# Kernel optimization log

Hardware: AMD Instinct MI355X
Metric: run time of the kernel (lower is better)

Reference implementation:

```python
import jax, jax.numpy as jnp
import numpy as np

N_NODES = 50000
N_GRAPHS = 256

def _gcn_layer(h, src, dst, W, b, n_nodes):
    # GCNConv: linear transform, add self-loops, symmetric deg^-1/2 norm, scatter-add, bias
    h = h @ W  # [N, C_out]
    loop = jnp.arange(n_nodes, dtype=src.dtype)
    src_f = jnp.concatenate([src, loop])
    dst_f = jnp.concatenate([dst, loop])
    ones = jnp.ones_like(dst_f, dtype=h.dtype)
    deg = jax.ops.segment_sum(ones, dst_f, num_segments=n_nodes)  # includes self-loops
    dinv = jnp.where(deg > 0, jax.lax.rsqrt(deg), 0.0)
    norm = dinv[src_f] * dinv[dst_f]  # [E+N]
    msg = h[src_f] * norm[:, None]
    out = jax.ops.segment_sum(msg, dst_f, num_segments=n_nodes)
    return out + b


def setup_inputs() -> dict:
    key = jax.random.key(0)
    ks = jax.random.split(key, 12)
    d_in, d_hid, nhid, nout = 128, 128, 256, 768
    x = jax.random.normal(ks[0], (N_NODES, d_in), dtype=jnp.float32)
    edge_index = jax.random.randint(ks[1], (2, 800000), 0, N_NODES, dtype=jnp.int64)
    batch = jnp.sort(jax.random.randint(ks[2], (N_NODES,), 0, N_GRAPHS, dtype=jnp.int64))
    def lin(k, fan_in, fan_out):
        lim = 1.0 / np.sqrt(fan_in)
        kw, kb = jax.random.split(k)
        W = jax.random.uniform(kw, (fan_in, fan_out), jnp.float32, -lim, lim)
        b = jax.random.uniform(kb, (fan_out,), jnp.float32, -lim, lim)
        return W, b
    W1, b1 = lin(ks[3], d_in, d_hid)
    W2, b2 = lin(ks[4], d_hid, d_hid)
    W3, b3 = lin(ks[5], d_hid, d_hid)
    Wm1, bm1 = lin(ks[6], d_hid, nhid)
    Wm2, bm2 = lin(ks[7], nhid, nout)
    return {"x": x, "edge_index": edge_index, "batch": batch,
            "W1": W1, "b1": b1, "W2": W2, "b2": b2, "W3": W3, "b3": b3,
            "Wm1": Wm1, "bm1": bm1, "Wm2": Wm2, "bm2": bm2}


def reference(x, edge_index, batch, W1, b1, W2, b2, W3, b3, Wm1, bm1, Wm2, bm2):
    src, dst = edge_index[0], edge_index[1]
    n = x.shape[0]
    h = jax.nn.relu(_gcn_layer(x, src, dst, W1, b1, n))
    h = jax.nn.relu(_gcn_layer(h, src, dst, W2, b2, n))
    h = _gcn_layer(h, src, dst, W3, b3, n)  # no relu before pooling (matches source)
    # global mean pool over graphs
    sums = jax.ops.segment_sum(h, batch, num_segments=N_GRAPHS)
    cnts = jax.ops.segment_sum(jnp.ones((n,), h.dtype), batch, num_segments=N_GRAPHS)
    pooled = sums / jnp.clip(cnts, 1.0)[:, None]  # [G, d_hid]
    out = jax.nn.relu(pooled @ Wm1 + bm1)
    out = out @ Wm2 + bm2  # [G, nout]
    return out
```

## Files before the change

kernel.cpp:

```cpp
#include <hip/hip_runtime.h>
#include <hip/hip_bf16.h>

using bf16 = __hip_bfloat16;
typedef __attribute__((ext_vector_type(8))) short bf16x8;
typedef __attribute__((ext_vector_type(4))) float f32x4;
typedef unsigned short u16;

__device__ __forceinline__ float lo2f(unsigned u) { return __uint_as_float(u << 16); }
__device__ __forceinline__ float hi2f(unsigned u) { return __uint_as_float(u & 0xffff0000u); }
__device__ __forceinline__ unsigned pack_bf2(float a, float b) {
    bf16 t0 = __float2bfloat16(a), t1 = __float2bfloat16(b);
    return (unsigned)*(unsigned short*)&t0 | ((unsigned)*(unsigned short*)&t1 << 16);
}

#define CAP 64
#define NPART 8
#define NCHUNK 256
#define PF 8

__global__ __launch_bounds__(256)
void fill_pad(const int* __restrict__ ei, int E, int N,
              int* __restrict__ cursor, u16* __restrict__ colPad)
{
    int part  = blockIdx.x & (NPART - 1);
    int chunk = blockIdx.x >> 3;
    int lo = (int)(((long long)N * part) >> 3);
    int hi = (int)(((long long)N * (part + 1)) >> 3);
    int csz = (E + NCHUNK - 1) / NCHUNK;
    int beg = chunk * csz;
    int end = min(beg + csz, E);
    const int* __restrict__ dstp = ei + E;
    for (int e0 = beg + (int)threadIdx.x; e0 < end; e0 += 256 * PF) {
        int dv[PF];
#pragma unroll
        for (int j = 0; j < PF; ++j) {
            int e = e0 + j * 256;
            dv[j] = (e < end) ? __builtin_nontemporal_load(dstp + e) : -1;
        }
#pragma unroll
        for (int j = 0; j < PF; ++j) {
            if (dv[j] >= lo && dv[j] < hi) {
                int e = e0 + j * 256;
                int s = __builtin_nontemporal_load(ei + e);
                int p = atomicAdd(&cursor[dv[j]], 1);
                if (p < CAP) colPad[(dv[j] << 6) + p] = (u16)s;
            }
        }
    }
}

__global__ __launch_bounds__(256)
void dinv_gstart(const int* __restrict__ cursor, int N, float* __restrict__ dinv,
                 const int* __restrict__ batch, int* __restrict__ gstart, int G,
                 u16* __restrict__ colPad, unsigned* __restrict__ gzero)
{
    int i = blockIdx.x * 256 + threadIdx.x;
    if (i < 64) gzero[i] = 0u;
    if (i >= N) return;
    int c = min(cursor[i], CAP);
    dinv[i] = rsqrtf((float)(c + 1));
    int pe = (c + 31) & ~31;
    if (pe > CAP) pe = CAP;
    for (int p = c; p < pe; ++p) colPad[(i << 6) + p] = (u16)N;
    int b = batch[i];
    int bp = (i == 0) ? -1 : batch[i - 1];
    for (int q = bp + 1; q <= b; ++q) gstart[q] = i;
    if (i == N - 1)
        for (int q = b + 1; q <= G; ++q) gstart[q] = N;
}

#define LDK 136

__global__ __launch_bounds__(256)
void gemm1_f32(const float* __restrict__ x, const float* __restrict__ W,
               const float* __restrict__ dinv, int N, bf16* __restrict__ g,
               int tiles)
{
    __shared__ short Wt[128 * LDK];
    for (int i = threadIdx.x; i < 128 * 128; i += 256) {
        int k = i >> 7, n = i & 127;
        bf16 b = __float2bfloat16(W[i]);
        Wt[n * LDK + k] = *(short*)&b;
    }
    __syncthreads();

    int wave = threadIdx.x >> 6;
    int lane = threadIdx.x & 63;
    int ln   = lane & 15;
    int quad = lane >> 4;

    for (int t = blockIdx.x; t < tiles; t += gridDim.x) {
        int m0 = t * 64 + wave * 16;
        if (m0 >= N) continue;

        int row = m0 + ln;
        if (row >= N) row = N - 1;
        const float* hrow = x + (size_t)row * 128;

        bf16x8 a[4];
#pragma unroll
        for (int kk = 0; kk < 4; ++kk) {
            float4 f0 = *(const float4*)(hrow + kk * 32 + quad * 8);
            float4 f1 = *(const float4*)(hrow + kk * 32 + quad * 8 + 4);
            float fv[8] = {f0.x, f0.y, f0.z, f0.w, f1.x, f1.y, f1.z, f1.w};
#pragma unroll
            for (int j = 0; j < 8; ++j) {
                bf16 tb = __float2bfloat16(fv[j]);
                ((short*)&a[kk])[j] = *(short*)&tb;
            }
        }

        f32x4 c[8];
#pragma unroll
        for (int nt = 0; nt < 8; ++nt) c[nt] = (f32x4){0.f, 0.f, 0.f, 0.f};
#pragma unroll
        for (int kk = 0; kk < 4; ++kk)
#pragma unroll
            for (int nt = 0; nt < 8; ++nt) {
                bf16x8 b = *(const bf16x8*)&Wt[(nt * 16 + ln) * LDK + kk * 32 + quad * 8];
                c[nt] = __builtin_amdgcn_mfma_f32_16x16x32_bf16(a[kk], b, c[nt], 0, 0, 0);
            }
#pragma unroll
        for (int r = 0; r < 4; ++r) {
            int m = m0 + quad * 4 + r;
            if (m < N) {
                float dv = dinv[m];
#pragma unroll
                for (int nt = 0; nt < 8; ++nt) {
                    bf16 val = __float2bfloat16(c[nt][r] * dv);
                    ((unsigned short*)g)[(size_t)m * 128 + nt * 16 + ln] = *(unsigned short*)&val;
                }
            }
        }
    }
}

__global__ __launch_bounds__(256)
void gemm_mfma(const bf16* __restrict__ hin, const float* __restrict__ W,
               const float* __restrict__ dinv, int N, bf16* __restrict__ g,
               int tiles)
{
    __shared__ short Wt[128 * LDK];
    for (int i = threadIdx.x; i < 128 * 128; i += 256) {
        int k = i >> 7, n = i & 127;
        bf16 b = __float2bfloat16(W[i]);
        Wt[n * LDK + k] = *(short*)&b;
    }
    __syncthreads();

    int wave = threadIdx.x >> 6;
    int lane = threadIdx.x & 63;
    int ln   = lane & 15;
    int quad = lane >> 4;

    for (int t = blockIdx.x; t < tiles; t += gridDim.x) {
        int m0 = t * 64 + wave * 16;
        if (m0 >= N) continue;

        int row = m0 + ln;
        if (row >= N) row = N - 1;
        const short* hrow = (const short*)hin + (size_t)row * 128;

        bf16x8 a[4];
#pragma unroll
        for (int kk = 0; kk < 4; ++kk)
            a[kk] = *(const bf16x8*)(hrow + kk * 32 + quad * 8);

        f32x4 c[8];
#pragma unroll
        for (int nt = 0; nt < 8; ++nt) c[nt] = (f32x4){0.f, 0.f, 0.f, 0.f};
#pragma unroll
        for (int kk = 0; kk < 4; ++kk)
#pragma unroll
            for (int nt = 0; nt < 8; ++nt) {
                bf16x8 b = *(const bf16x8*)&Wt[(nt * 16 + ln) * LDK + kk * 32 + quad * 8];
                c[nt] = __builtin_amdgcn_mfma_f32_16x16x32_bf16(a[kk], b, c[nt], 0, 0, 0);
            }
#pragma unroll
        for (int r = 0; r < 4; ++r) {
            int m = m0 + quad * 4 + r;
            if (m < N) {
                float dv = dinv[m];
#pragma unroll
                for (int nt = 0; nt < 8; ++nt) {
                    bf16 val = __float2bfloat16(c[nt][r] * dv);
                    ((unsigned short*)g)[(size_t)m * 128 + nt * 16 + ln] = *(unsigned short*)&val;
                }
            }
        }
    }
}

__global__ __launch_bounds__(256)
void gather16(const bf16* __restrict__ g, const int* __restrict__ cnt,
              const u16* __restrict__ colPad, const float* __restrict__ dinv,
              const float* __restrict__ bias, int N, int do_relu, bf16* __restrict__ hout)
{
    int v = blockIdx.x * 4 + (threadIdx.x >> 6);
    if (v >= N) return;
    int lane = threadIdx.x & 63;
    const unsigned* gp = (const unsigned*)g;

    unsigned su = gp[(size_t)v * 64 + lane];
    float s0 = lo2f(su), s1 = hi2f(su);

    int beg = v << 6;
    int c = min(cnt[v], CAP);
    int pe = (c + 31) & ~31;
    if (pe > CAP) pe = CAP;
    int end = beg + pe;
    for (int i = beg; i < end; i += 32) {
        int4 cp0 = *(const int4*)(colPad + i);
        int4 cp1 = *(const int4*)(colPad + i + 8);
        int4 cp2 = *(const int4*)(colPad + i + 16);
        int4 cp3 = *(const int4*)(colPad + i + 24);
        int cc[32] = {
            cp0.x & 0xffff, (cp0.x >> 16) & 0xffff, cp0.y & 0xffff, (cp0.y >> 16) & 0xffff,
            cp0.z & 0xffff, (cp0.z >> 16) & 0xffff, cp0.w & 0xffff, (cp0.w >> 16) & 0xffff,
            cp1.x & 0xffff, (cp1.x >> 16) & 0xffff, cp1.y & 0xffff, (cp1.y >> 16) & 0xffff,
            cp1.z & 0xffff, (cp1.z >> 16) & 0xffff, cp1.w & 0xffff, (cp1.w >> 16) & 0xffff,
            cp2.x & 0xffff, (cp2.x >> 16) & 0xffff, cp2.y & 0xffff, (cp2.y >> 16) & 0xffff,
            cp2.z & 0xffff, (cp2.z >> 16) & 0xffff, cp2.w & 0xffff, (cp2.w >> 16) & 0xffff,
            cp3.x & 0xffff, (cp3.x >> 16) & 0xffff, cp3.y & 0xffff, (cp3.y >> 16) & 0xffff,
            cp3.z & 0xffff, (cp3.z >> 16) & 0xffff, cp3.w & 0xffff, (cp3.w >> 16) & 0xffff };
        unsigned uu[32];
#pragma unroll
        for (int j = 0; j < 32; ++j) uu[j] = gp[(size_t)cc[j] * 64 + lane];
#pragma unroll
        for (int j = 0; j < 32; ++j) { s0 += lo2f(uu[j]); s1 += hi2f(uu[j]); }
    }
    float dv = dinv[v];
    float2 bb = ((const float2*)bias)[lane];
    float r0 = fmaf(dv, s0, bb.x);
    float r1 = fmaf(dv, s1, bb.y);
    if (do_relu) { r0 = fmaxf(r0, 0.f); r1 = fmaxf(r1, 0.f); }
    ((unsigned*)hout)[(size_t)v * 64 + lane] = pack_bf2(r0, r1);
}

#define PCH 16
__global__ __launch_bounds__(64)
void pool_part(const bf16* __restrict__ h, const int* __restrict__ batch, int N,
               float* __restrict__ pooled)
{
    int c0 = blockIdx.x * PCH;
    if (c0 >= N) return;
    int t = threadIdx.x;
    int end = min(c0 + PCH, N);
    int cur = batch[c0];
    float a0 = 0.f, a1 = 0.f;
    const unsigned* hp = (const unsigned*)h;
    for (int v = c0; v < end; ++v) {
        int b = batch[v];
        if (b != cur) {
            atomicAdd(&pooled[cur * 128 + 2 * t], a0);
            atomicAdd(&pooled[cur * 128 + 2 * t + 1], a1);
            a0 = a1 = 0.f;
            cur = b;
        }
        unsigned u = hp[(size_t)v * 64 + t];
        a0 += lo2f(u);
        a1 += hi2f(u);
    }
    atomicAdd(&pooled[cur * 128 + 2 * t], a0);
    atomicAdd(&pooled[cur * 128 + 2 * t + 1], a1);
}

__global__ __launch_bounds__(256)
void mlp1g(const float* __restrict__ pooled, const int* __restrict__ gstart,
           const float* __restrict__ Wm1, const float* __restrict__ bm1,
           float* __restrict__ O)
{
    __shared__ float Ps[128];
    int gg = blockIdx.x, j = threadIdx.x;
    if (j < 128) {
        int c = gstart[gg + 1] - gstart[gg];
        Ps[j] = pooled[gg * 128 + j] / (float)(c > 0 ? c : 1);
    }
    __syncthreads();
    float s = 0.f;
#pragma unroll 4
    for (int k = 0; k < 128; ++k) s = fmaf(Ps[k], Wm1[k * 256 + j], s);
    O[(size_t)gg * 256 + j] = fmaxf(s + bm1[j], 0.f);
}

__global__ __launch_bounds__(768)
void mlp2g(const float* __restrict__ O, const float* __restrict__ Wm2,
           const float* __restrict__ bm2, float* __restrict__ out)
{
    __shared__ float Os[256];
    int gg = blockIdx.x, j = threadIdx.x;
    if (j < 256) Os[j] = O[(size_t)gg * 256 + j];
    __syncthreads();
    float s = 0.f;
#pragma unroll 4
    for (int k = 0; k < 256; ++k) s = fmaf(Os[k], Wm2[k * 768 + j], s);
    out[(size_t)gg * 768 + j] = s + bm2[j];
}

extern "C" void kernel_launch(void* const* d_in, const int* in_sizes, int n_in,
                              void* d_out, int out_size, void* d_ws, size_t ws_size,
                              hipStream_t stream)
{
    const float* x     = (const float*)d_in[0];
    const int*   ei    = (const int*)d_in[1];
    const int*   batch = (const int*)d_in[2];
    const float *W1 = (const float*)d_in[3],  *bb1 = (const float*)d_in[4];
    const float *W2 = (const float*)d_in[5],  *bb2 = (const float*)d_in[6];
    const float *W3 = (const float*)d_in[7],  *bb3 = (const float*)d_in[8];
    const float *Wm1 = (const float*)d_in[9],  *bm1 = (const float*)d_in[10];
    const float *Wm2 = (const float*)d_in[11], *bm2 = (const float*)d_in[12];

    const int N = in_sizes[2];
    const int E = in_sizes[1] / 2;
    const int G = out_size / 768;

    char* wp = (char*)d_ws;
    bf16* bufG   = (bf16*)wp;  wp += (size_t)(N + 1) * 128 * 2;
    bf16* bufH   = (bf16*)wp;  wp += (size_t)N * 128 * 2;
    u16*  colPad = (u16*)wp;   wp += (size_t)N * CAP * 2;
    int*  cursor = (int*)wp;   wp += (size_t)N * 4;
    float* pooled= (float*)wp; wp += (size_t)G * 128 * 4;
    float* dinv  = (float*)wp; wp += (size_t)N * 4;
    int*  gstart = (int*)wp;   wp += (size_t)(G + 1) * 4;
    float* Obuf  = (float*)wp; wp += (size_t)G * 256 * 4;

    hipMemsetAsync(cursor, 0, (size_t)N * 4 + (size_t)G * 128 * 4, stream);

    const int SB = (N + 255) / 256;
    const int gemm_tiles  = (N + 63) / 64;
    const int gemm_grid   = (gemm_tiles + 1) / 2;
    const int gather_grid = (N + 3) / 4;

    fill_pad<<<NPART * NCHUNK, 256, 0, stream>>>(ei, E, N, cursor, colPad);
    dinv_gstart<<<SB, 256, 0, stream>>>(cursor, N, dinv, batch, gstart, G,
                                        colPad, (unsigned*)bufG + (size_t)N * 64);

    gemm1_f32<<<gemm_grid, 256, 0, stream>>>(x, W1, dinv, N, bufG, gemm_tiles);
    gather16<<<gather_grid, 256, 0, stream>>>(bufG, cursor, colPad, dinv, bb1, N, 1, bufH);
    gemm_mfma<<<gemm_grid, 256, 0, stream>>>(bufH, W2, dinv, N, bufG, gemm_tiles);
    gather16<<<gather_grid, 256, 0, stream>>>(bufG, cursor, colPad, dinv, bb2, N, 1, bufH);
    gemm_mfma<<<gemm_grid, 256, 0, stream>>>(bufH, W3, dinv, N, bufG, gemm_tiles);
    gather16<<<gather_grid, 256, 0, stream>>>(bufG, cursor, colPad, dinv, bb3, N, 0, bufH);

    pool_part<<<(N + PCH - 1) / PCH, 64, 0, stream>>>(bufH, batch, N, pooled);
    mlp1g<<<G, 256, 0, stream>>>(pooled, gstart, Wm1, bm1, Obuf);
    mlp2g<<<G, 768, 0, stream>>>(Obuf, Wm2, bm2, (float*)d_out);
}
```

Baseline: 307.3 us.

## Fuse mean-pool into last gather and merge the two MLP kernels

The final gather now atomically adds each node's output directly into the per-graph pooled buffer instead of writing bf16 node features that a separate pool kernel re-reads. The two MLP head kernels are merged into one kernel, with the hidden activation kept in shared memory. This removes two launches, an intermediate buffer write/read and a global hidden buffer. In exchange, atomic traffic rises sharply (one atomic per node-feature instead of per 16-node chunk), with heavy contention on same-graph addresses.

```diff
diff --git a/kernel.cpp b/kernel.cpp
--- a/kernel.cpp
+++ b/kernel.cpp
@@ -194,7 +194,8 @@
 __global__ __launch_bounds__(256)
 void gather16(const bf16* __restrict__ g, const int* __restrict__ cnt,
               const u16* __restrict__ colPad, const float* __restrict__ dinv,
-              const float* __restrict__ bias, int N, int do_relu, bf16* __restrict__ hout)
+              const float* __restrict__ bias, int N, int do_relu, bf16* __restrict__ hout,
+              const int* __restrict__ batch, float* __restrict__ pooled, int do_pool)
 {
     int v = blockIdx.x * 4 + (threadIdx.x >> 6);
     if (v >= N) return;
@@ -234,62 +235,35 @@
     float r0 = fmaf(dv, s0, bb.x);
     float r1 = fmaf(dv, s1, bb.y);
     if (do_relu) { r0 = fmaxf(r0, 0.f); r1 = fmaxf(r1, 0.f); }
-    ((unsigned*)hout)[(size_t)v * 64 + lane] = pack_bf2(r0, r1);
-}
-
-#define PCH 16
-__global__ __launch_bounds__(64)
-void pool_part(const bf16* __restrict__ h, const int* __restrict__ batch, int N,
-               float* __restrict__ pooled)
-{
-    int c0 = blockIdx.x * PCH;
-    if (c0 >= N) return;
-    int t = threadIdx.x;
-    int end = min(c0 + PCH, N);
-    int cur = batch[c0];
-    float a0 = 0.f, a1 = 0.f;
-    const unsigned* hp = (const unsigned*)h;
-    for (int v = c0; v < end; ++v) {
+    if (do_pool) {
         int b = batch[v];
-        if (b != cur) {
-            atomicAdd(&pooled[cur * 128 + 2 * t], a0);
-            atomicAdd(&pooled[cur * 128 + 2 * t + 1], a1);
-            a0 = a1 = 0.f;
-            cur = b;
-        }
-        unsigned u = hp[(size_t)v * 64 + t];
-        a0 += lo2f(u);
-        a1 += hi2f(u);
-    }
-    atomicAdd(&pooled[cur * 128 + 2 * t], a0);
-    atomicAdd(&pooled[cur * 128 + 2 * t + 1], a1);
-}
-
-__global__ __launch_bounds__(256)
-void mlp1g(const float* __restrict__ pooled, const int* __restrict__ gstart,
-           const float* __restrict__ Wm1, const float* __restrict__ bm1,
-           float* __restrict__ O)
+        atomicAdd(&pooled[b * 128 + 2 * lane], r0);
+        atomicAdd(&pooled[b * 128 + 2 * lane + 1], r1);
+    } else {
+        ((unsigned*)hout)[(size_t)v * 64 + lane] = pack_bf2(r0, r1);
+    }
+}
+
+__global__ __launch_bounds__(768)
+void mlp_fused(const float* __restrict__ pooled, const int* __restrict__ gstart,
+               const float* __restrict__ Wm1, const float* __restrict__ bm1,
+               const float* __restrict__ Wm2, const float* __restrict__ bm2,
+               float* __restrict__ out)
 {
     __shared__ float Ps[128];
+    __shared__ float Os[256];
     int gg = blockIdx.x, j = threadIdx.x;
     if (j < 128) {
         int c = gstart[gg + 1] - gstart[gg];
         Ps[j] = pooled[gg * 128 + j] / (float)(c > 0 ? c : 1);
     }
     __syncthreads();
-    float s = 0.f;
+    if (j < 256) {
+        float s = 0.f;
 #pragma unroll 4
-    for (int k = 0; k < 128; ++k) s = fmaf(Ps[k], Wm1[k * 256 + j], s);
-    O[(size_t)gg * 256 + j] = fmaxf(s + bm1[j], 0.f);
-}
-
-__global__ __launch_bounds__(768)
-void mlp2g(const float* __restrict__ O, const float* __restrict__ Wm2,
-           const float* __restrict__ bm2, float* __restrict__ out)
-{
-    __shared__ float Os[256];
-    int gg = blockIdx.x, j = threadIdx.x;
-    if (j < 256) Os[j] = O[(size_t)gg * 256 + j];
+        for (int k = 0; k < 128; ++k) s = fmaf(Ps[k], Wm1[k * 256 + j], s);
+        Os[j] = fmaxf(s + bm1[j], 0.f);
+    }
     __syncthreads();
     float s = 0.f;
 #pragma unroll 4
@@ -322,7 +296,6 @@
     float* pooled= (float*)wp; wp += (size_t)G * 128 * 4;
     float* dinv  = (float*)wp; wp += (size_t)N * 4;
     int*  gstart = (int*)wp;   wp += (size_t)(G + 1) * 4;
-    float* Obuf  = (float*)wp; wp += (size_t)G * 256 * 4;
 
     hipMemsetAsync(cursor, 0, (size_t)N * 4 + (size_t)G * 128 * 4, stream);
 
@@ -336,13 +309,14 @@
                                         colPad, (unsigned*)bufG + (size_t)N * 64);
 
     gemm1_f32<<<gemm_grid, 256, 0, stream>>>(x, W1, dinv, N, bufG, gemm_tiles);
-    gather16<<<gather_grid, 256, 0, stream>>>(bufG, cursor, colPad, dinv, bb1, N, 1, bufH);
+    gather16<<<gather_grid, 256, 0, stream>>>(bufG, cursor, colPad, dinv, bb1, N, 1,
+                                              bufH, batch, pooled, 0);
     gemm_mfma<<<gemm_grid, 256, 0, stream>>>(bufH, W2, dinv, N, bufG, gemm_tiles);
-    gather16<<<gather_grid, 256, 0, stream>>>(bufG, cursor, colPad, dinv, bb2, N, 1, bufH);
+    gather16<<<gather_grid, 256, 0, stream>>>(bufG, cursor, colPad, dinv, bb2, N, 1,
+                                              bufH, batch, pooled, 0);
     gemm_mfma<<<gemm_grid, 256, 0, stream>>>(bufH, W3, dinv, N, bufG, gemm_tiles);
-    gather16<<<gather_grid, 256, 0, stream>>>(bufG, cursor, colPad, dinv, bb3, N, 0, bufH);
-
-    pool_part<<<(N + PCH - 1) / PCH, 64, 0, stream>>>(bufH, batch, N, pooled);
-    mlp1g<<<G, 256, 0, stream>>>(pooled, gstart, Wm1, bm1, Obuf);
-    mlp2g<<<G, 768, 0, stream>>>(Obuf, Wm2, bm2, (float*)d_out);
-}
+    gather16<<<gather_grid, 256, 0, stream>>>(bufG, cursor, colPad, dinv, bb3, N, 0,
+                                              bufH, batch, pooled, 1);
+
+    mlp_fused<<<G, 768, 0, stream>>>(pooled, gstart, Wm1, bm1, Wm2, bm2, (float*)d_out);
+}
```

Result: slower. 330.9 us (+7.7%).
